# Optimization experiments

Hardware: AMD Instinct MI355X
Metric: run time of the kernel (lower is better)

The kernel has to match this reference:

```python
import jax, jax.numpy as jnp
import numpy as np


def setup_inputs() -> dict:
    key = jax.random.key(0)
    k1, k2, k3 = jax.random.split(key, 3)
    B, F, K = 16384, 512, 1000
    D = jax.random.normal(k1, (B, F), dtype=jnp.float32)
    weight = jax.random.normal(k2, (K, F), dtype=jnp.float32)  # (out_features, in_features)
    gamma = jax.random.uniform(k3, (K,), dtype=jnp.float32)
    return {"D": D, "weight": weight, "gamma": gamma}


def reference(D, weight, gamma):
    # Squared Euclidean distance from each row of D to each centroid (row of weight),
    # computed via ||a||^2 + ||b||^2 - 2 a.b (mathematically equal to the broadcast
    # subtract-square-sum in the original torch forward with d_view=None).
    d_sq = jnp.sum(D * D, axis=1, keepdims=True)            # (B, 1)
    w_sq = jnp.sum(weight * weight, axis=1)                  # (K,)
    cross = jnp.einsum('bf,kf->bk', D, weight)               # (B, K)
    dist_sq = d_sq + w_sq[None, :] - 2.0 * cross             # (B, K)
    return -dist_sq * gamma                                  # (B, K)
```

## Files before the change

kernel.cpp:

```cpp
#include <hip/hip_runtime.h>
#include <hip/hip_bf16.h>
#include <stdint.h>

#define B_ROWS 16384
#define F_DIM  512
#define K_OUT  1000
#define K_PAD  1024

#define BM 128
#define BN 128
#define BK 64

typedef __attribute__((ext_vector_type(4))) float f32x4;
typedef __attribute__((ext_vector_type(8))) short short8;
typedef unsigned short u16;
typedef unsigned int   u32;

#define OFF_DB   0
#define OFF_WB   16777216
#define OFF_DSQ  (16777216 + 1048576)
#define OFF_WSQ  (16777216 + 1048576 + 65536)

__device__ __forceinline__ u16 f2bf(float f) {
  union { float f; u32 u; } v; v.f = f;
  u32 u = v.u;
  u32 r = (u + 0x7fffu + ((u >> 16) & 1u)) >> 16;
  return (u16)r;
}

__global__ void prep(const float* __restrict__ D, const float* __restrict__ W,
                     u16* __restrict__ Db, u16* __restrict__ Wb,
                     float* __restrict__ dsq, float* __restrict__ wsq) {
  int w    = threadIdx.x >> 6;
  int lane = threadIdx.x & 63;
  if (blockIdx.x < B_ROWS / 4) {
    int row = blockIdx.x * 4 + w;
    const float* src = D + (size_t)row * F_DIM + lane * 8;
    float4 v0 = *(const float4*)src;
    float4 v1 = *(const float4*)(src + 4);
    float s = v0.x*v0.x + v0.y*v0.y + v0.z*v0.z + v0.w*v0.w
            + v1.x*v1.x + v1.y*v1.y + v1.z*v1.z + v1.w*v1.w;
#pragma unroll
    for (int off = 32; off >= 1; off >>= 1) s += __shfl_xor(s, off);
    if (lane == 0) dsq[row] = s;
    uint4 p;
    p.x = (u32)f2bf(v0.x) | ((u32)f2bf(v0.y) << 16);
    p.y = (u32)f2bf(v0.z) | ((u32)f2bf(v0.w) << 16);
    p.z = (u32)f2bf(v1.x) | ((u32)f2bf(v1.y) << 16);
    p.w = (u32)f2bf(v1.z) | ((u32)f2bf(v1.w) << 16);
    *(uint4*)(Db + (size_t)row * F_DIM + lane * 8) = p;
  } else {
    int row = (blockIdx.x - B_ROWS / 4) * 4 + w;
    uint4 p; p.x = p.y = p.z = p.w = 0u;
    float s = 0.f;
    if (row < K_OUT) {
      const float* src = W + (size_t)row * F_DIM + lane * 8;
      float4 v0 = *(const float4*)src;
      float4 v1 = *(const float4*)(src + 4);
      s = v0.x*v0.x + v0.y*v0.y + v0.z*v0.z + v0.w*v0.w
        + v1.x*v1.x + v1.y*v1.y + v1.z*v1.z + v1.w*v1.w;
      p.x = (u32)f2bf(v0.x) | ((u32)f2bf(v0.y) << 16);
      p.y = (u32)f2bf(v0.z) | ((u32)f2bf(v0.w) << 16);
      p.z = (u32)f2bf(v1.x) | ((u32)f2bf(v1.y) << 16);
      p.w = (u32)f2bf(v1.z) | ((u32)f2bf(v1.w) << 16);
    }
#pragma unroll
    for (int off = 32; off >= 1; off >>= 1) s += __shfl_xor(s, off);
    if (lane == 0) wsq[row] = s;
    *(uint4*)(Wb + (size_t)row * F_DIM + lane * 8) = p;
  }
}

__device__ __forceinline__ void gload_lds16(const void* g, void* l) {
  __builtin_amdgcn_global_load_lds(
      (const __attribute__((address_space(1))) void*)g,
      (__attribute__((address_space(3))) void*)l,
      16, 0, 0);
}


#define READ_A(QM)                                                             \
  _Pragma("unroll") for (int mi2 = 0; mi2 < 2; ++mi2)                          \
  _Pragma("unroll") for (int kk = 0; kk < 2; ++kk) {                           \
    int r = wm * 64 + (QM) * 32 + mi2 * 16 + lr;                               \
    a[mi2][kk] = *(const short8*)(sAc + r * 128 +                              \
                                  ((((kk << 2) + lk4) ^ (r & 7)) << 4));       \
  }

#define READ_B(QN)                                                             \
  _Pragma("unroll") for (int ni2 = 0; ni2 < 2; ++ni2)                          \
  _Pragma("unroll") for (int kk = 0; kk < 2; ++kk) {                           \
    int r = wn * 64 + (QN) * 32 + ni2 * 16 + lr;                               \
    b[ni2][kk] = *(const short8*)(sBc + r * 128 +                              \
                                  ((((kk << 2) + lk4) ^ (r & 7)) << 4));       \
  }

#define STAGE_A(h)                                                             \
  _Pragma("unroll") for (int j = 0; j < 2; ++j) {                              \
    int rb = (h) * 32 + j * 64 + w * 8;                                        \
    int r  = rb + (lane >> 3);                                                 \
    int sc = s8 ^ (r & 7);                                                     \
    gload_lds16(Ag + (size_t)r * F_DIM + kbn + sc * 8, sAn + rb * 128);        \
  }

#define STAGE_B(q)                                                             \
  _Pragma("unroll") for (int j = 0; j < 2; ++j) {                              \
    int rb = (q) * 32 + j * 64 + w * 8;                                        \
    int r  = rb + (lane >> 3);                                                 \
    int sc = s8 ^ (r & 7);                                                     \
    gload_lds16(Bg + (size_t)r * F_DIM + kbn + sc * 8, sBn + rb * 128);        \
  }

#define MFMA_Q(QM, QN)                                                         \
  asm volatile("s_waitcnt lgkmcnt(0)" ::: "memory");                           \
  __builtin_amdgcn_sched_barrier(0);                                           \
  __builtin_amdgcn_s_setprio(1);                                               \
  _Pragma("unroll") for (int mi2 = 0; mi2 < 2; ++mi2)                          \
  _Pragma("unroll") for (int ni2 = 0; ni2 < 2; ++ni2)                          \
  _Pragma("unroll") for (int kk = 0; kk < 2; ++kk)                             \
    acc[(QM)*2 + mi2][(QN)*2 + ni2] =                                          \
        __builtin_amdgcn_mfma_f32_16x16x32_bf16(                               \
            a[mi2][kk], b[ni2][kk], acc[(QM)*2 + mi2][(QN)*2 + ni2], 0, 0, 0); \
  __builtin_amdgcn_s_setprio(0);                                               \
  __builtin_amdgcn_s_barrier();

#define VM6  asm volatile("s_waitcnt vmcnt(6)" ::: "memory")
#define BAR  __builtin_amdgcn_s_barrier()

__global__ __launch_bounds__(256, 2) void gemm_eps(
    const u16* __restrict__ A,
    const u16* __restrict__ Bw,
    const float* __restrict__ dsq,
    const float* __restrict__ wsq,
    const float* __restrict__ gamma,
    float* __restrict__ out) {
  __shared__ __align__(16) char lds[65536];

  const int tid  = threadIdx.x;
  const int w    = tid >> 6;
  const int lane = tid & 63;
  const int lr   = lane & 15;
  const int lk4  = lane >> 4;
  const int wm   = w >> 1;
  const int wn   = w & 1;

  const int bid = blockIdx.x;
  const int wg  = (bid & 7) * 128 + (bid >> 3);
  const int mt  = wg >> 3;
  const int nt  = wg & 7;
  const int m0  = mt * BM;
  const int n0  = nt * BN;

  const u16* Ag = A  + (size_t)m0 * F_DIM;
  const u16* Bg = Bw + (size_t)n0 * F_DIM;

  const int s8 = lane & 7;

  f32x4 acc[4][4];
#pragma unroll
  for (int i = 0; i < 4; ++i)
#pragma unroll
    for (int j = 0; j < 4; ++j) acc[i][j] = (f32x4){0.f, 0.f, 0.f, 0.f};

  {
    char* sAn = lds;
    char* sBn = lds + 16384;
    const int kbn = 0;
    STAGE_A(0) STAGE_B(0) STAGE_B(1) STAGE_A(1)
  }

#pragma unroll 2
  for (int t = 0; t < 8; ++t) {
    char* sAc = lds + (t & 1) * 32768;
    char* sBc = sAc + 16384;
    char* sAn = lds + ((t + 1) & 1) * 32768;
    char* sBn = sAn + 16384;
    const int kbn = ((t + 1) & 7) * BK;
    short8 a[2][2], b[2][2];

    STAGE_A(0) VM6; BAR;
    READ_A(0) READ_B(0)
    MFMA_Q(0, 0)
    STAGE_B(0) VM6; BAR;
    READ_B(1)
    MFMA_Q(0, 1)
    STAGE_B(1) VM6; BAR;
    READ_A(1)
    MFMA_Q(1, 1)
    STAGE_A(1) BAR;
    READ_B(0)
    MFMA_Q(1, 0)
  }

  float g_[4], wq_[4];
#pragma unroll
  for (int ni = 0; ni < 4; ++ni) {
    int col = n0 + wn * 64 + ni * 16 + lr;
    g_[ni]  = (col < K_OUT) ? gamma[col] : 0.f;
    wq_[ni] = (col < K_OUT) ? wsq[col]   : 0.f;
  }
  float* ch = (float*)lds;
  const int rl = tid >> 3;
  const int cb = (tid & 7) << 2;
#pragma unroll
  for (int c = 0; c < 2; ++c) {
    __syncthreads();
    if (wm == c) {
#pragma unroll
      for (int mi = 0; mi < 4; ++mi) {
        const int row_l = mi * 16 + lk4 * 4;
        const int grow  = m0 + c * 64 + row_l;
#pragma unroll
        for (int j = 0; j < 4; ++j) {
          float dq = dsq[grow + j];
#pragma unroll
          for (int ni = 0; ni < 4; ++ni) {
            ch[(row_l + j) * 132 + wn * 64 + ni * 16 + lr] =
                g_[ni] * (2.f * acc[mi][ni][j] - dq - wq_[ni]);
          }
        }
      }
    }
    __syncthreads();
#pragma unroll
    for (int half = 0; half < 2; ++half) {
#pragma unroll
      for (int s = 0; s < 4; ++s) {
        int row = half * 32 + rl;
        int col = cb + s * 32;
        if (n0 + col < K_OUT) {
          float4 v = *(const float4*)&ch[row * 132 + col];
          *(float4*)&out[(size_t)(m0 + c * 64 + row) * K_OUT + n0 + col] = v;
        }
      }
    }
  }
}

extern "C" void kernel_launch(void* const* d_in, const int* in_sizes, int n_in,
                              void* d_out, int out_size, void* d_ws, size_t ws_size,
                              hipStream_t stream) {
  const float* D     = (const float*)d_in[0];
  const float* W     = (const float*)d_in[1];
  const float* gamma = (const float*)d_in[2];
  float* out = (float*)d_out;
  char*  ws  = (char*)d_ws;

  u16*   Db  = (u16*)(ws + OFF_DB);
  u16*   Wb  = (u16*)(ws + OFF_WB);
  float* dsq = (float*)(ws + OFF_DSQ);
  float* wsq = (float*)(ws + OFF_WSQ);

  prep<<<B_ROWS / 4 + K_PAD / 4, 256, 0, stream>>>(D, W, Db, Wb, dsq, wsq);

  gemm_eps<<<(B_ROWS / BM) * (K_PAD / BN), 256, 0, stream>>>(
      Db, Wb, dsq, wsq, gamma, out);
}
```

Baseline: 40.48 us.

## Replace quadrant-interleaved K loop with single-barrier full-tile MFMA schedule

Replaces the four-phase quadrant pipeline (staging A/B halves interleaved with MFMA quadrants and four barriers per K step) with a simpler loop. It issues all next-tile global->LDS loads, waits once with vmcnt(8), reads every A/B fragment for the tile from LDS, then runs all 32 MFMAs back to back at raised priority. This cuts the barriers per K step from four to two and gives the scheduler a larger MFMA block. In exchange it holds more fragment registers (16 short8 instead of 8) and overlaps LDS reads less finely with MFMA work. It also moves the gamma, wsq and dsq loads before the main loop, with dsq read as vectorised float4, so their latency is hidden behind the GEMM.

```diff
diff --git a/kernel.cpp b/kernel.cpp
--- a/kernel.cpp
+++ b/kernel.cpp
@@ -79,22 +79,6 @@
 }
 
 
-#define READ_A(QM)                                                             \
-  _Pragma("unroll") for (int mi2 = 0; mi2 < 2; ++mi2)                          \
-  _Pragma("unroll") for (int kk = 0; kk < 2; ++kk) {                           \
-    int r = wm * 64 + (QM) * 32 + mi2 * 16 + lr;                               \
-    a[mi2][kk] = *(const short8*)(sAc + r * 128 +                              \
-                                  ((((kk << 2) + lk4) ^ (r & 7)) << 4));       \
-  }
-
-#define READ_B(QN)                                                             \
-  _Pragma("unroll") for (int ni2 = 0; ni2 < 2; ++ni2)                          \
-  _Pragma("unroll") for (int kk = 0; kk < 2; ++kk) {                           \
-    int r = wn * 64 + (QN) * 32 + ni2 * 16 + lr;                               \
-    b[ni2][kk] = *(const short8*)(sBc + r * 128 +                              \
-                                  ((((kk << 2) + lk4) ^ (r & 7)) << 4));       \
-  }
-
 #define STAGE_A(h)                                                             \
   _Pragma("unroll") for (int j = 0; j < 2; ++j) {                              \
     int rb = (h) * 32 + j * 64 + w * 8;                                        \
@@ -110,22 +94,6 @@
     int sc = s8 ^ (r & 7);                                                     \
     gload_lds16(Bg + (size_t)r * F_DIM + kbn + sc * 8, sBn + rb * 128);        \
   }
-
-#define MFMA_Q(QM, QN)                                                         \
-  asm volatile("s_waitcnt lgkmcnt(0)" ::: "memory");                           \
-  __builtin_amdgcn_sched_barrier(0);                                           \
-  __builtin_amdgcn_s_setprio(1);                                               \
-  _Pragma("unroll") for (int mi2 = 0; mi2 < 2; ++mi2)                          \
-  _Pragma("unroll") for (int ni2 = 0; ni2 < 2; ++ni2)                          \
-  _Pragma("unroll") for (int kk = 0; kk < 2; ++kk)                             \
-    acc[(QM)*2 + mi2][(QN)*2 + ni2] =                                          \
-        __builtin_amdgcn_mfma_f32_16x16x32_bf16(                               \
-            a[mi2][kk], b[ni2][kk], acc[(QM)*2 + mi2][(QN)*2 + ni2], 0, 0, 0); \
-  __builtin_amdgcn_s_setprio(0);                                               \
-  __builtin_amdgcn_s_barrier();
-
-#define VM6  asm volatile("s_waitcnt vmcnt(6)" ::: "memory")
-#define BAR  __builtin_amdgcn_s_barrier()
 
 __global__ __launch_bounds__(256, 2) void gemm_eps(
     const u16* __restrict__ A,
@@ -162,11 +130,23 @@
 #pragma unroll
     for (int j = 0; j < 4; ++j) acc[i][j] = (f32x4){0.f, 0.f, 0.f, 0.f};
 
+  float g_[4], wq_[4];
+  float4 dl[4];
+#pragma unroll
+  for (int ni = 0; ni < 4; ++ni) {
+    int col = n0 + wn * 64 + ni * 16 + lr;
+    g_[ni]  = (col < K_OUT) ? gamma[col] : 0.f;
+    wq_[ni] = wsq[col & (K_PAD - 1)];
+  }
+#pragma unroll
+  for (int mi = 0; mi < 4; ++mi)
+    dl[mi] = *(const float4*)&dsq[m0 + wm * 64 + mi * 16 + lk4 * 4];
+
   {
     char* sAn = lds;
     char* sBn = lds + 16384;
     const int kbn = 0;
-    STAGE_A(0) STAGE_B(0) STAGE_B(1) STAGE_A(1)
+    STAGE_A(0) STAGE_A(1) STAGE_B(0) STAGE_B(1)
   }
 
 #pragma unroll 2
@@ -176,29 +156,41 @@
     char* sAn = lds + ((t + 1) & 1) * 32768;
     char* sBn = sAn + 16384;
     const int kbn = ((t + 1) & 7) * BK;
-    short8 a[2][2], b[2][2];
-
-    STAGE_A(0) VM6; BAR;
-    READ_A(0) READ_B(0)
-    MFMA_Q(0, 0)
-    STAGE_B(0) VM6; BAR;
-    READ_B(1)
-    MFMA_Q(0, 1)
-    STAGE_B(1) VM6; BAR;
-    READ_A(1)
-    MFMA_Q(1, 1)
-    STAGE_A(1) BAR;
-    READ_B(0)
-    MFMA_Q(1, 0)
-  }
-
-  float g_[4], wq_[4];
-#pragma unroll
-  for (int ni = 0; ni < 4; ++ni) {
-    int col = n0 + wn * 64 + ni * 16 + lr;
-    g_[ni]  = (col < K_OUT) ? gamma[col] : 0.f;
-    wq_[ni] = (col < K_OUT) ? wsq[col]   : 0.f;
-  }
+
+    STAGE_A(0) STAGE_A(1) STAGE_B(0) STAGE_B(1)
+
+    asm volatile("s_waitcnt vmcnt(8)" ::: "memory");
+    __builtin_amdgcn_s_barrier();
+    asm volatile("" ::: "memory");
+
+    short8 a[2][4], b[2][4];
+#pragma unroll
+    for (int kk = 0; kk < 2; ++kk)
+#pragma unroll
+      for (int mi = 0; mi < 4; ++mi) {
+        int rA = wm * 64 + mi * 16 + lr;
+        a[kk][mi] = *(const short8*)(sAc + rA * 128 +
+                                     ((((kk << 2) + lk4) ^ (rA & 7)) << 4));
+        int rB = wn * 64 + mi * 16 + lr;
+        b[kk][mi] = *(const short8*)(sBc + rB * 128 +
+                                     ((((kk << 2) + lk4) ^ (rB & 7)) << 4));
+      }
+
+    __builtin_amdgcn_s_setprio(1);
+#pragma unroll
+    for (int kk = 0; kk < 2; ++kk)
+#pragma unroll
+      for (int mi = 0; mi < 4; ++mi)
+#pragma unroll
+        for (int ni = 0; ni < 4; ++ni)
+          acc[mi][ni] = __builtin_amdgcn_mfma_f32_16x16x32_bf16(
+              a[kk][mi], b[kk][ni], acc[mi][ni], 0, 0, 0);
+    __builtin_amdgcn_s_setprio(0);
+
+    asm volatile("" ::: "memory");
+    __builtin_amdgcn_s_barrier();
+  }
+
   float* ch = (float*)lds;
   const int rl = tid >> 3;
   const int cb = (tid & 7) << 2;
@@ -209,10 +201,10 @@
 #pragma unroll
       for (int mi = 0; mi < 4; ++mi) {
         const int row_l = mi * 16 + lk4 * 4;
-        const int grow  = m0 + c * 64 + row_l;
 #pragma unroll
         for (int j = 0; j < 4; ++j) {
-          float dq = dsq[grow + j];
+          float dq = (j == 0) ? dl[mi].x : (j == 1) ? dl[mi].y
+                   : (j == 2) ? dl[mi].z : dl[mi].w;
 #pragma unroll
           for (int ni = 0; ni < 4; ++ni) {
             ch[(row_l + j) * 132 + wn * 64 + ni * 16 + lr] =
```

After: 39.73 us. No clear change (-1.8%).
